# Kernel tuning notes

Hardware: AMD Instinct MI355X
Metric: run time of the kernel (lower is better)

The kernel has to match this reference:

```python
import jax, jax.numpy as jnp
import numpy as np

B, S, D, H = 16, 2048, 2048, 16
HD = D // H
PROJ = D  # proj_ratio = 1.0
PAD_ID = 50257
LN_EPS = 1e-5
MASKED_BIAS = -1e9


def setup_inputs() -> dict:
    key = jax.random.key(0)
    ks = jax.random.split(key, 12)
    sc = 0.02
    return {
        "hidden_states": jax.random.normal(ks[0], (B, S, D), dtype=jnp.float32),
        "input_ids_with_pads": jax.random.randint(ks[1], (B, S), 0, PAD_ID, dtype=jnp.int64),
        "ln_w": jnp.ones((D,), jnp.float32),
        "ln_b": jnp.zeros((D,), jnp.float32),
        "wq": sc * jax.random.normal(ks[2], (D, D), jnp.float32),
        "bq": jnp.zeros((D,), jnp.float32),
        "wk": sc * jax.random.normal(ks[3], (D, D), jnp.float32),
        "bk": jnp.zeros((D,), jnp.float32),
        "wv": sc * jax.random.normal(ks[4], (D, D), jnp.float32),
        "bv": jnp.zeros((D,), jnp.float32),
        "wo": sc * jax.random.normal(ks[5], (D, PROJ), jnp.float32),
        "bo": jnp.zeros((PROJ,), jnp.float32),
    }


def _layernorm(x, g, b):
    mu = jnp.mean(x, axis=-1, keepdims=True)
    var = jnp.mean(jnp.square(x - mu), axis=-1, keepdims=True)
    return (x - mu) * jax.lax.rsqrt(var + LN_EPS) * g + b


def _last_token_index(tokens):
    # select_at_last_token: argmax of cumsum of the non-pad mask == index of
    # the last non-pad token (first index where the cumsum reaches its max).
    mask = (tokens != PAD_ID).astype(jnp.int32)
    return jnp.argmax(jnp.cumsum(mask, axis=1), axis=1)  # [B]


def reference(hidden_states, input_ids_with_pads, ln_w, ln_b,
              wq, bq, wk, bk, wv, bv, wo, bo):
    x = _layernorm(hidden_states, ln_w, ln_b)  # [B,S,D]
    idx = _last_token_index(input_ids_with_pads)
    # Efficient gather instead of the original index_select + diagonal trick.
    x_last = x[jnp.arange(B), idx]  # [B,D]

    q = (x_last @ wq + bq).reshape(B, H, HD)          # single query per batch
    k = (x @ wk + bk).reshape(B, S, H, HD).transpose(0, 2, 1, 3)  # [B,H,S,HD]
    v = (x @ wv + bv).reshape(B, S, H, HD).transpose(0, 2, 1, 3)  # [B,H,S,HD]

    # GPT-Neo _attn: compute in float32, NO 1/sqrt(head_dim) scaling.
    # Causal mask for query at position key_length-1 covers the full key range,
    # i.e. it is all-True here, so it is a no-op (kept implicit).
    w = jnp.einsum("bhd,bhsd->bhs", q.astype(jnp.float32), k.astype(jnp.float32))
    w = jax.nn.softmax(w, axis=-1).astype(v.dtype)    # [B,H,S]
    attn = jnp.einsum("bhs,bhsd->bhd", w, v)          # [B,H,HD]
    attn = attn.reshape(B, D)                          # merge heads
    out = attn @ wo + bo                               # [B,PROJ]
    return out
```

## Files before the change

kernel.cpp:

```cpp
#include <hip/hip_runtime.h>
#include <hip/hip_bf16.h>

#define BB 16
#define SS 2048
#define DD 2048
#define HH 16
#define HDIM 128
#define PAD_ID 50257
#define LN_EPS 1e-5f

__device__ __forceinline__ float block_sum256(float v, float* s4) {
    #pragma unroll
    for (int m = 32; m >= 1; m >>= 1) v += __shfl_xor(v, m, 64);
    __syncthreads();
    if ((threadIdx.x & 63) == 0) s4[threadIdx.x >> 6] = v;
    __syncthreads();
    return s4[0] + s4[1] + s4[2] + s4[3];
}
__device__ __forceinline__ float block_max256(float v, float* s4) {
    #pragma unroll
    for (int m = 32; m >= 1; m >>= 1) v = fmaxf(v, __shfl_xor(v, m, 64));
    __syncthreads();
    if ((threadIdx.x & 63) == 0) s4[threadIdx.x >> 6] = v;
    __syncthreads();
    return fmaxf(fmaxf(s4[0], s4[1]), fmaxf(s4[2], s4[3]));
}

__device__ __forceinline__ void gl16(const float* g, float* l) {
    __builtin_amdgcn_global_load_lds(
        (const __attribute__((address_space(1))) void*)g,
        (__attribute__((address_space(3))) void*)l,
        16, 0, 0);
}

__global__ __launch_bounds__(256) void k_prep(const float* __restrict__ hid, const int* __restrict__ ids,
                                              const float* __restrict__ g, const float* __restrict__ be,
                                              float* __restrict__ xlast) {
    int b = blockIdx.x, t = threadIdx.x;
    __shared__ int sm[256];
    __shared__ float s4[4];
    const int* row = ids + (size_t)b * SS;
    int best = -1;
    for (int s = t; s < SS; s += 256)
        if (row[s] != PAD_ID) best = s;
    sm[t] = best;
    __syncthreads();
    for (int off = 128; off > 0; off >>= 1) {
        if (t < off) sm[t] = max(sm[t], sm[t + off]);
        __syncthreads();
    }
    int idx = (sm[0] < 0) ? 0 : sm[0];
    const float4* row4 = (const float4*)(hid + ((size_t)b * SS + idx) * DD);
    float4 v0 = row4[t], v1 = row4[t + 256];
    float s  = v0.x + v0.y + v0.z + v0.w + v1.x + v1.y + v1.z + v1.w;
    float sq = v0.x*v0.x + v0.y*v0.y + v0.z*v0.z + v0.w*v0.w
             + v1.x*v1.x + v1.y*v1.y + v1.z*v1.z + v1.w*v1.w;
    s  = block_sum256(s, s4);
    sq = block_sum256(sq, s4);
    float mu = s * (1.0f / DD);
    float rstd = rsqrtf(sq * (1.0f / DD) - mu * mu + LN_EPS);
    const float4* g4 = (const float4*)g;
    const float4* b4 = (const float4*)be;
    float4 ga = g4[t], gb = g4[t + 256], ba = b4[t], bb = b4[t + 256];
    float4 o0, o1;
    o0.x = (v0.x - mu) * rstd * ga.x + ba.x;  o0.y = (v0.y - mu) * rstd * ga.y + ba.y;
    o0.z = (v0.z - mu) * rstd * ga.z + ba.z;  o0.w = (v0.w - mu) * rstd * ga.w + ba.w;
    o1.x = (v1.x - mu) * rstd * gb.x + bb.x;  o1.y = (v1.y - mu) * rstd * gb.y + bb.y;
    o1.z = (v1.z - mu) * rstd * gb.z + bb.z;  o1.w = (v1.w - mu) * rstd * gb.w + bb.w;
    ((float4*)(xlast + (size_t)b * DD))[t]       = o0;
    ((float4*)(xlast + (size_t)b * DD))[t + 256] = o1;
}

__global__ __launch_bounds__(256) void k_init3(float* __restrict__ q, float* __restrict__ attn,
                                               float* __restrict__ out, const float* __restrict__ bq,
                                               const float* __restrict__ bv, const float* __restrict__ bo) {
    int i = blockIdx.x * 256 + threadIdx.x;
    int which = blockIdx.y;
    float* dst = which == 0 ? q : (which == 1 ? attn : out);
    const float* bias = which == 0 ? bq : (which == 1 ? bv : bo);
    dst[i] = bias[i & (DD - 1)];
}

__global__ __launch_bounds__(256) void k_q(const float* __restrict__ xlast, const float* __restrict__ wq,
                                           float* __restrict__ q) {
    int ptile = blockIdx.x, kch = blockIdx.y, tid = threadIdx.x;
    __shared__ float xs[16][64];
    {
        int b = tid >> 4, c4 = tid & 15;
        *(float4*)&xs[b][c4 * 4] = *(const float4*)&xlast[(size_t)b * DD + kch * 64 + c4 * 4];
    }
    __syncthreads();
    int p = ptile * 256 + tid;
    float acc[16];
    #pragma unroll
    for (int b = 0; b < 16; b++) acc[b] = 0.f;
    for (int dd = 0; dd < 64; dd++) {
        float wqv = wq[(size_t)(kch * 64 + dd) * DD + p];
        #pragma unroll
        for (int b = 0; b < 16; b++) acc[b] = fmaf(xs[b][dd], wqv, acc[b]);
    }
    #pragma unroll
    for (int b = 0; b < 16; b++) atomicAdd(&q[(size_t)b * DD + p], acc[b]);
}

__global__ __launch_bounds__(256) void k_t(const float* __restrict__ wk, const float* __restrict__ q,
                                           const float* __restrict__ g, float* __restrict__ t_out,
                                           float* __restrict__ tg_out) {
    int d = blockIdx.x, tid = threadIdx.x;
    __shared__ float wkl[16 * 132];
    #pragma unroll
    for (int k = 0; k < 2; k++) {
        int f4 = tid + k * 256;
        int h = f4 >> 5, j4 = f4 & 31;
        *(float4*)&wkl[h * 132 + j4 * 4] = *(const float4*)&wk[(size_t)d * DD + h * 128 + j4 * 4];
    }
    __syncthreads();
    int b = tid >> 4, h = tid & 15;
    const float4* q4 = (const float4*)(q + (size_t)b * DD + h * 128);
    float acc = 0.f;
    #pragma unroll
    for (int j4 = 0; j4 < 32; j4++) {
        float4 qv = q4[j4];
        float4 wv4 = *(const float4*)&wkl[h * 132 + j4 * 4];
        acc = fmaf(qv.x, wv4.x, fmaf(qv.y, wv4.y, fmaf(qv.z, wv4.z, fmaf(qv.w, wv4.w, acc))));
    }
    size_t o = (size_t)(b * 16 + h) * DD + d;
    t_out[o] = acc;
    tg_out[o] = acc * g[d];
}

__global__ __launch_bounds__(256) void k_G(const float* __restrict__ t_in, const float* __restrict__ tg_in,
                                           const float* __restrict__ q, const float* __restrict__ lnb,
                                           const float* __restrict__ bk, float* __restrict__ G1,
                                           float* __restrict__ wconst) {
    int bh = blockIdx.x, tid = threadIdx.x;
    int b = bh >> 4, h = bh & 15;
    __shared__ float s4[4];
    const float4* tg4 = (const float4*)(tg_in + (size_t)bh * DD);
    const float4* t4  = (const float4*)(t_in + (size_t)bh * DD);
    const float4* lb4 = (const float4*)lnb;
    float g1p = 0.f, g2p = 0.f;
    #pragma unroll
    for (int k = 0; k < 2; k++) {
        int f = tid + k * 256;
        float4 a = tg4[f];
        g1p += a.x + a.y + a.z + a.w;
        float4 tv = t4[f];
        float4 bv = lb4[f];
        g2p = fmaf(tv.x, bv.x, fmaf(tv.y, bv.y, fmaf(tv.z, bv.z, fmaf(tv.w, bv.w, g2p))));
    }
    float cp = 0.f;
    if (tid < 128) cp = bk[h * 128 + tid] * q[(size_t)b * DD + h * 128 + tid];
    float G1v = block_sum256(g1p, s4);
    float rest = block_sum256(g2p + cp, s4);
    if (tid == 0) { G1[bh] = G1v; wconst[bh] = rest; }
}

__global__ __launch_bounds__(256) void k_logits8(const float* __restrict__ hid, const float* __restrict__ tg,
                                                 const float* __restrict__ G1, const float* __restrict__ wcst,
                                                 float* __restrict__ wout, float* __restrict__ muA,
                                                 float* __restrict__ rsA) {
    __shared__ float smem[12288];
    int b = blockIdx.x, st = blockIdx.y;
    int tid = threadIdx.x, qd = tid & 15, rp = tid >> 4;
    const float* hb = hid + ((size_t)b * SS + st * 32) * DD;
    const float* tgb = tg + (size_t)b * 16 * DD;

    float raw[2][16], sum[2], ssq[2];
    #pragma unroll
    for (int r = 0; r < 2; r++) {
        sum[r] = 0.f; ssq[r] = 0.f;
        #pragma unroll
        for (int h = 0; h < 16; h++) raw[r][h] = 0.f;
    }

    auto stage = [&](int c, int buf) {
        int d0 = c * 128;
        float* xd = smem + buf * 4096;
        float* td = smem + 8192 + buf * 2048;
        #pragma unroll
        for (int i = 0; i < 4; i++) {
            int f = i * 256 + tid;
            int row = f >> 5, c4 = f & 31;
            gl16(&hb[(size_t)row * DD + d0 + c4 * 4], &xd[f * 4]);
        }
        #pragma unroll
        for (int i = 0; i < 2; i++) {
            int f = i * 256 + tid;
            int h = f >> 5, c4 = f & 31;
            gl16(&tgb[(size_t)h * DD + d0 + c4 * 4], &td[f * 4]);
        }
    };

    stage(0, 0);
    __syncthreads();

    int cur = 0;
    #pragma unroll 1
    for (int c = 0; c < 16; c++) {
        if (c < 15) stage(c + 1, cur ^ 1);
        const float* xb = smem + cur * 4096;
        const float* tb = smem + 8192 + cur * 2048;
        #pragma unroll
        for (int k = 0; k < 2; k++) {
            float4 x0 = *(const float4*)&xb[(rp * 2 + 0) * 128 + (qd + 16 * k) * 4];
            float4 x1 = *(const float4*)&xb[(rp * 2 + 1) * 128 + (qd + 16 * k) * 4];
            #pragma unroll
            for (int h = 0; h < 16; h++) {
                float4 tv = *(const float4*)&tb[h * 128 + (qd + 16 * k) * 4];
                raw[0][h] = fmaf(x0.x, tv.x, fmaf(x0.y, tv.y, fmaf(x0.z, tv.z, fmaf(x0.w, tv.w, raw[0][h]))));
                raw[1][h] = fmaf(x1.x, tv.x, fmaf(x1.y, tv.y, fmaf(x1.z, tv.z, fmaf(x1.w, tv.w, raw[1][h]))));
            }
            sum[0] += x0.x + x0.y + x0.z + x0.w;
            sum[1] += x1.x + x1.y + x1.z + x1.w;
            ssq[0] = fmaf(x0.x, x0.x, fmaf(x0.y, x0.y, fmaf(x0.z, x0.z, fmaf(x0.w, x0.w, ssq[0]))));
            ssq[1] = fmaf(x1.x, x1.x, fmaf(x1.y, x1.y, fmaf(x1.z, x1.z, fmaf(x1.w, x1.w, ssq[1]))));
        }
        __syncthreads();
        cur ^= 1;
    }

    #pragma unroll
    for (int m = 1; m < 16; m <<= 1) {
        #pragma unroll
        for (int r = 0; r < 2; r++) {
            sum[r] += __shfl_xor(sum[r], m, 64);
            ssq[r] += __shfl_xor(ssq[r], m, 64);
        }
    }

    float g1 = G1[b * 16 + qd];
    float wc = wcst[b * 16 + qd];
    float* red = smem;
    #pragma unroll
    for (int rr = 0; rr < 2; rr++) {
        __syncthreads();
        #pragma unroll
        for (int h = 0; h < 16; h++) red[tid * 17 + h] = raw[rr][h];
        __syncthreads();
        float tot = 0.f;
        #pragma unroll
        for (int j = 0; j < 16; j++) tot += red[(rp * 16 + j) * 17 + qd];
        int s = st * 32 + rp * 2 + rr;
        float mu = sum[rr] * (1.0f / DD);
        float rstd = rsqrtf(ssq[rr] * (1.0f / DD) - mu * mu + LN_EPS);
        wout[(size_t)(b * 16 + qd) * SS + s] = rstd * (tot - mu * g1) + wc;
        if (qd == 0) { muA[(size_t)b * SS + s] = mu; rsA[(size_t)b * SS + s] = rstd; }
    }
}

__global__ __launch_bounds__(256) void k_softmax(const float* __restrict__ wlog, const float* __restrict__ muA,
                                                 const float* __restrict__ rsA, float* __restrict__ coef,
                                                 float* __restrict__ Mout) {
    int bh = blockIdx.x, tid = threadIdx.x;
    int b = bh >> 4;
    __shared__ float s4[4];
    const float4* w4 = (const float4*)(wlog + (size_t)bh * SS);
    float4 v0 = w4[tid], v1 = w4[tid + 256];
    float mx = fmaxf(fmaxf(fmaxf(v0.x, v0.y), fmaxf(v0.z, v0.w)),
                     fmaxf(fmaxf(v1.x, v1.y), fmaxf(v1.z, v1.w)));
    mx = block_max256(mx, s4);
    float4 e0, e1;
    e0.x = __expf(v0.x - mx); e0.y = __expf(v0.y - mx); e0.z = __expf(v0.z - mx); e0.w = __expf(v0.w - mx);
    e1.x = __expf(v1.x - mx); e1.y = __expf(v1.y - mx); e1.z = __expf(v1.z - mx); e1.w = __expf(v1.w - mx);
    float ssum = e0.x + e0.y + e0.z + e0.w + e1.x + e1.y + e1.z + e1.w;
    ssum = block_sum256(ssum, s4);
    float inv = 1.0f / ssum;
    const float4* r4 = (const float4*)(rsA + (size_t)b * SS);
    const float4* m4 = (const float4*)(muA + (size_t)b * SS);
    float4 ra = r4[tid], rb = r4[tid + 256], ma = m4[tid], mb = m4[tid + 256];
    float4 c0, c1;
    c0.x = e0.x * inv * ra.x; c0.y = e0.y * inv * ra.y; c0.z = e0.z * inv * ra.z; c0.w = e0.w * inv * ra.w;
    c1.x = e1.x * inv * rb.x; c1.y = e1.y * inv * rb.y; c1.z = e1.z * inv * rb.z; c1.w = e1.w * inv * rb.w;
    ((float4*)(coef + (size_t)bh * SS))[tid] = c0;
    ((float4*)(coef + (size_t)bh * SS))[tid + 256] = c1;
    float Mp = c0.x * ma.x + c0.y * ma.y + c0.z * ma.z + c0.w * ma.w
             + c1.x * mb.x + c1.y * mb.y + c1.z * mb.z + c1.w * mb.w;
    Mp = block_sum256(Mp, s4);
    if (tid == 0) Mout[bh] = Mp;
}

__global__ __launch_bounds__(256) void k_pv6(const float* __restrict__ hid, const float* __restrict__ coef,
                                             float* __restrict__ Apart) {
    int b = blockIdx.x, dt = blockIdx.y, ch = blockIdx.z, tid = threadIdx.x;
    __shared__ float cl[128][16];
    int s0 = ch * 128;
    #pragma unroll
    for (int k = 0; k < 2; k++) {
        int f = tid + k * 256; int h = f >> 5, s4i = f & 31;
        float4 c4 = *(const float4*)&coef[(size_t)(b * 16 + h) * SS + s0 + s4i * 4];
        cl[s4i * 4 + 0][h] = c4.x; cl[s4i * 4 + 1][h] = c4.y;
        cl[s4i * 4 + 2][h] = c4.z; cl[s4i * 4 + 3][h] = c4.w;
    }
    __syncthreads();
    int d = dt * 1024 + tid * 4;
    const float* hb = hid + ((size_t)b * SS + s0) * DD + d;
    float4 acc[16];
    #pragma unroll
    for (int h = 0; h < 16; h++) acc[h] = make_float4(0.f, 0.f, 0.f, 0.f);
    float4 xv[8];
    #pragma unroll
    for (int i = 0; i < 8; i++) xv[i] = *(const float4*)(hb + (size_t)i * DD);
    #pragma unroll 1
    for (int sb = 0; sb < 16; sb++) {
        #pragma unroll
        for (int i = 0; i < 8; i++) {
            int s = sb * 8 + i;
            float4 x = xv[i];
            if (sb < 15) xv[i] = *(const float4*)(hb + (size_t)(s + 8) * DD);
            float4 ca = *(const float4*)&cl[s][0];
            float4 cb = *(const float4*)&cl[s][4];
            float4 cc = *(const float4*)&cl[s][8];
            float4 cd = *(const float4*)&cl[s][12];
            acc[0].x = fmaf(ca.x, x.x, acc[0].x); acc[0].y = fmaf(ca.x, x.y, acc[0].y);
            acc[0].z = fmaf(ca.x, x.z, acc[0].z); acc[0].w = fmaf(ca.x, x.w, acc[0].w);
            acc[1].x = fmaf(ca.y, x.x, acc[1].x); acc[1].y = fmaf(ca.y, x.y, acc[1].y);
            acc[1].z = fmaf(ca.y, x.z, acc[1].z); acc[1].w = fmaf(ca.y, x.w, acc[1].w);
            acc[2].x = fmaf(ca.z, x.x, acc[2].x); acc[2].y = fmaf(ca.z, x.y, acc[2].y);
            acc[2].z = fmaf(ca.z, x.z, acc[2].z); acc[2].w = fmaf(ca.z, x.w, acc[2].w);
            acc[3].x = fmaf(ca.w, x.x, acc[3].x); acc[3].y = fmaf(ca.w, x.y, acc[3].y);
            acc[3].z = fmaf(ca.w, x.z, acc[3].z); acc[3].w = fmaf(ca.w, x.w, acc[3].w);
            acc[4].x = fmaf(cb.x, x.x, acc[4].x); acc[4].y = fmaf(cb.x, x.y, acc[4].y);
            acc[4].z = fmaf(cb.x, x.z, acc[4].z); acc[4].w = fmaf(cb.x, x.w, acc[4].w);
            acc[5].x = fmaf(cb.y, x.x, acc[5].x); acc[5].y = fmaf(cb.y, x.y, acc[5].y);
            acc[5].z = fmaf(cb.y, x.z, acc[5].z); acc[5].w = fmaf(cb.y, x.w, acc[5].w);
            acc[6].x = fmaf(cb.z, x.x, acc[6].x); acc[6].y = fmaf(cb.z, x.y, acc[6].y);
            acc[6].z = fmaf(cb.z, x.z, acc[6].z); acc[6].w = fmaf(cb.z, x.w, acc[6].w);
            acc[7].x = fmaf(cb.w, x.x, acc[7].x); acc[7].y = fmaf(cb.w, x.y, acc[7].y);
            acc[7].z = fmaf(cb.w, x.z, acc[7].z); acc[7].w = fmaf(cb.w, x.w, acc[7].w);
            acc[8].x = fmaf(cc.x, x.x, acc[8].x); acc[8].y = fmaf(cc.x, x.y, acc[8].y);
            acc[8].z = fmaf(cc.x, x.z, acc[8].z); acc[8].w = fmaf(cc.x, x.w, acc[8].w);
            acc[9].x = fmaf(cc.y, x.x, acc[9].x); acc[9].y = fmaf(cc.y, x.y, acc[9].y);
            acc[9].z = fmaf(cc.y, x.z, acc[9].z); acc[9].w = fmaf(cc.y, x.w, acc[9].w);
            acc[10].x = fmaf(cc.z, x.x, acc[10].x); acc[10].y = fmaf(cc.z, x.y, acc[10].y);
            acc[10].z = fmaf(cc.z, x.z, acc[10].z); acc[10].w = fmaf(cc.z, x.w, acc[10].w);
            acc[11].x = fmaf(cc.w, x.x, acc[11].x); acc[11].y = fmaf(cc.w, x.y, acc[11].y);
            acc[11].z = fmaf(cc.w, x.z, acc[11].z); acc[11].w = fmaf(cc.w, x.w, acc[11].w);
            acc[12].x = fmaf(cd.x, x.x, acc[12].x); acc[12].y = fmaf(cd.x, x.y, acc[12].y);
            acc[12].z = fmaf(cd.x, x.z, acc[12].z); acc[12].w = fmaf(cd.x, x.w, acc[12].w);
            acc[13].x = fmaf(cd.y, x.x, acc[13].x); acc[13].y = fmaf(cd.y, x.y, acc[13].y);
            acc[13].z = fmaf(cd.y, x.z, acc[13].z); acc[13].w = fmaf(cd.y, x.w, acc[13].w);
            acc[14].x = fmaf(cd.z, x.x, acc[14].x); acc[14].y = fmaf(cd.z, x.y, acc[14].y);
            acc[14].z = fmaf(cd.z, x.z, acc[14].z); acc[14].w = fmaf(cd.z, x.w, acc[14].w);
            acc[15].x = fmaf(cd.w, x.x, acc[15].x); acc[15].y = fmaf(cd.w, x.y, acc[15].y);
            acc[15].z = fmaf(cd.w, x.z, acc[15].z); acc[15].w = fmaf(cd.w, x.w, acc[15].w);
        }
    }
    #pragma unroll
    for (int h = 0; h < 16; h++)
        *(float4*)&Apart[((size_t)(ch * 16 + b) * 16 + h) * DD + d] = acc[h];
}

__global__ __launch_bounds__(256) void k_attnv(const float* __restrict__ Apart, const float* __restrict__ M,
                                               const float* __restrict__ g, const float* __restrict__ be,
                                               const float* __restrict__ wv, float* __restrict__ attn) {
    int h = blockIdx.x, dc = blockIdx.y, tid = threadIdx.x;
    __shared__ float yl[16][64];
    int d0 = dc * 64;
    {
        int b = tid >> 4, c4 = tid & 15;
        float4 a4 = make_float4(0.f, 0.f, 0.f, 0.f);
        #pragma unroll
        for (int ch = 0; ch < 16; ch++) {
            float4 v = *(const float4*)&Apart[((size_t)(ch * 16 + b) * 16 + h) * DD + d0 + c4 * 4];
            a4.x += v.x; a4.y += v.y; a4.z += v.z; a4.w += v.w;
        }
        float4 g4 = *(const float4*)&g[d0 + c4 * 4];
        float4 b4 = *(const float4*)&be[d0 + c4 * 4];
        float m = M[b * 16 + h];
        float4 y;
        y.x = g4.x * (a4.x - m) + b4.x;  y.y = g4.y * (a4.y - m) + b4.y;
        y.z = g4.z * (a4.z - m) + b4.z;  y.w = g4.w * (a4.w - m) + b4.w;
        *(float4*)&yl[b][c4 * 4] = y;
    }
    __syncthreads();
    int j = tid & 127, h2 = tid >> 7;
    float acc[16];
    #pragma unroll
    for (int b = 0; b < 16; b++) acc[b] = 0.f;
    for (int dl = 0; dl < 32; dl++) {
        int dd = h2 * 32 + dl;
        float wvv = wv[(size_t)(d0 + dd) * DD + h * 128 + j];
        #pragma unroll
        for (int b = 0; b < 16; b++) acc[b] = fmaf(yl[b][dd], wvv, acc[b]);
    }
    #pragma unroll
    for (int b = 0; b < 16; b++) atomicAdd(&attn[(size_t)b * DD + h * 128 + j], acc[b]);
}

__global__ __launch_bounds__(256) void k_out(const float* __restrict__ attn, const float* __restrict__ wo,
                                             float* __restrict__ out) {
    int ptile = blockIdx.x, cch = blockIdx.y, tid = threadIdx.x;
    __shared__ float al[16][64];
    int c0 = cch * 64;
    {
        int b = tid >> 4, c4 = tid & 15;
        *(float4*)&al[b][c4 * 4] = *(const float4*)&attn[(size_t)b * DD + c0 + c4 * 4];
    }
    __syncthreads();
    int p = ptile * 256 + tid;
    float acc[16];
    #pragma unroll
    for (int b = 0; b < 16; b++) acc[b] = 0.f;
    for (int cc = 0; cc < 64; cc++) {
        float wov = wo[(size_t)(c0 + cc) * DD + p];
        #pragma unroll
        for (int b = 0; b < 16; b++) acc[b] = fmaf(al[b][cc], wov, acc[b]);
    }
    #pragma unroll
    for (int b = 0; b < 16; b++) atomicAdd(&out[(size_t)b * DD + p], acc[b]);
}

extern "C" void kernel_launch(void* const* d_in, const int* in_sizes, int n_in,
                              void* d_out, int out_size, void* d_ws, size_t ws_size,
                              hipStream_t stream) {
    const float* hid = (const float*)d_in[0];
    const int*   ids = (const int*)d_in[1];
    const float* lnw = (const float*)d_in[2];
    const float* lnb = (const float*)d_in[3];
    const float* wq  = (const float*)d_in[4];
    const float* bq  = (const float*)d_in[5];
    const float* wk  = (const float*)d_in[6];
    const float* bk  = (const float*)d_in[7];
    const float* wv  = (const float*)d_in[8];
    const float* bv  = (const float*)d_in[9];
    const float* wo  = (const float*)d_in[10];
    const float* bo  = (const float*)d_in[11];
    float* out = (float*)d_out;

    float* ws = (float*)d_ws;
    float* xlast = ws;
    float* q     = xlast + 32768;
    float* t     = q + 32768;
    float* tg    = t + 524288;
    float* G1    = tg + 524288;
    float* wcst  = G1 + 256;
    float* wlog  = wcst + 256;
    float* muA   = wlog + 524288;
    float* rsA   = muA + 32768;
    float* coef  = rsA + 32768;
    float* Mbh   = coef + 524288;
    float* Abh   = Mbh + 256;
    float* attn  = Abh + 524288;
    float* Apart = attn + 32768;

    k_prep<<<16, 256, 0, stream>>>(hid, ids, lnw, lnb, xlast);
    k_init3<<<dim3(128, 3), 256, 0, stream>>>(q, attn, out, bq, bv, bo);
    k_q<<<dim3(8, 32), 256, 0, stream>>>(xlast, wq, q);
    k_t<<<2048, 256, 0, stream>>>(wk, q, lnw, t, tg);
    k_G<<<256, 256, 0, stream>>>(t, tg, q, lnb, bk, G1, wcst);
    k_logits8<<<dim3(16, 64), 256, 0, stream>>>(hid, tg, G1, wcst, wlog, muA, rsA);
    k_softmax<<<256, 256, 0, stream>>>(wlog, muA, rsA, coef, Mbh);
    k_pv6<<<dim3(16, 2, 16), 256, 0, stream>>>(hid, coef, Apart);
    k_attnv<<<dim3(16, 32), 256, 0, stream>>>(Apart, Mbh, lnw, lnb, wv, attn);
    k_out<<<dim3(8, 32), 256, 0, stream>>>(attn, wo, out);
}
```

Measured before the change: 222.6 us.

## Retile logits kernel to 8 rows by 4 heads per thread

Changes the per-thread register tile in the logits kernel from 2 sequence rows × 16 heads to 8 rows × 4 heads. Each thread now loads 4 head vectors and 8 row vectors per step, which changes the ratio of LDS traffic to FMAs. The cross-lane reduction moves from a padded shared-memory transpose to shuffle reductions, followed by a small shared-memory scatter for the output. Only one head group computes the LayerNorm statistics, so the redundant sum and sum-of-squares work is dropped. The tradeoff is many more shuffle reductions per thread and more divergent branching.

```diff
diff --git a/kernel.cpp b/kernel.cpp
--- a/kernel.cpp
+++ b/kernel.cpp
@@ -156,22 +156,23 @@
     if (tid == 0) { G1[bh] = G1v; wconst[bh] = rest; }
 }
 
-__global__ __launch_bounds__(256) void k_logits8(const float* __restrict__ hid, const float* __restrict__ tg,
-                                                 const float* __restrict__ G1, const float* __restrict__ wcst,
-                                                 float* __restrict__ wout, float* __restrict__ muA,
-                                                 float* __restrict__ rsA) {
+__global__ __launch_bounds__(256) void k_logits13(const float* __restrict__ hid, const float* __restrict__ tg,
+                                                  const float* __restrict__ G1, const float* __restrict__ wcst,
+                                                  float* __restrict__ wout, float* __restrict__ muA,
+                                                  float* __restrict__ rsA) {
     __shared__ float smem[12288];
     int b = blockIdx.x, st = blockIdx.y;
-    int tid = threadIdx.x, qd = tid & 15, rp = tid >> 4;
+    int tid = threadIdx.x, qd = tid & 15, g = tid >> 4;
+    int sg = g & 3, hg = g >> 2;
     const float* hb = hid + ((size_t)b * SS + st * 32) * DD;
     const float* tgb = tg + (size_t)b * 16 * DD;
 
-    float raw[2][16], sum[2], ssq[2];
-    #pragma unroll
-    for (int r = 0; r < 2; r++) {
+    float raw[8][4], sum[8], ssq[8];
+    #pragma unroll
+    for (int r = 0; r < 8; r++) {
         sum[r] = 0.f; ssq[r] = 0.f;
         #pragma unroll
-        for (int h = 0; h < 16; h++) raw[r][h] = 0.f;
+        for (int h = 0; h < 4; h++) raw[r][h] = 0.f;
     }
 
     auto stage = [&](int c, int buf) {
@@ -203,18 +204,33 @@
         const float* tb = smem + 8192 + cur * 2048;
         #pragma unroll
         for (int k = 0; k < 2; k++) {
-            float4 x0 = *(const float4*)&xb[(rp * 2 + 0) * 128 + (qd + 16 * k) * 4];
-            float4 x1 = *(const float4*)&xb[(rp * 2 + 1) * 128 + (qd + 16 * k) * 4];
+            float4 tv0 = *(const float4*)&tb[(hg * 4 + 0) * 128 + (qd + 16 * k) * 4];
+            float4 tv1 = *(const float4*)&tb[(hg * 4 + 1) * 128 + (qd + 16 * k) * 4];
+            float4 tv2 = *(const float4*)&tb[(hg * 4 + 2) * 128 + (qd + 16 * k) * 4];
+            float4 tv3 = *(const float4*)&tb[(hg * 4 + 3) * 128 + (qd + 16 * k) * 4];
             #pragma unroll
-            for (int h = 0; h < 16; h++) {
-                float4 tv = *(const float4*)&tb[h * 128 + (qd + 16 * k) * 4];
-                raw[0][h] = fmaf(x0.x, tv.x, fmaf(x0.y, tv.y, fmaf(x0.z, tv.z, fmaf(x0.w, tv.w, raw[0][h]))));
-                raw[1][h] = fmaf(x1.x, tv.x, fmaf(x1.y, tv.y, fmaf(x1.z, tv.z, fmaf(x1.w, tv.w, raw[1][h]))));
+            for (int half = 0; half < 2; half++) {
+                float4 xr[4];
+                #pragma unroll
+                for (int r2 = 0; r2 < 4; r2++)
+                    xr[r2] = *(const float4*)&xb[(sg * 8 + half * 4 + r2) * 128 + (qd + 16 * k) * 4];
+                #pragma unroll
+                for (int r2 = 0; r2 < 4; r2++) {
+                    float4 x = xr[r2];
+                    raw[half * 4 + r2][0] = fmaf(x.x, tv0.x, fmaf(x.y, tv0.y, fmaf(x.z, tv0.z, fmaf(x.w, tv0.w, raw[half * 4 + r2][0]))));
+                    raw[half * 4 + r2][1] = fmaf(x.x, tv1.x, fmaf(x.y, tv1.y, fmaf(x.z, tv1.z, fmaf(x.w, tv1.w, raw[half * 4 + r2][1]))));
+                    raw[half * 4 + r2][2] = fmaf(x.x, tv2.x, fmaf(x.y, tv2.y, fmaf(x.z, tv2.z, fmaf(x.w, tv2.w, raw[half * 4 + r2][2]))));
+                    raw[half * 4 + r2][3] = fmaf(x.x, tv3.x, fmaf(x.y, tv3.y, fmaf(x.z, tv3.z, fmaf(x.w, tv3.w, raw[half * 4 + r2][3]))));
+                }
+                if (hg == 0) {
+                    #pragma unroll
+                    for (int r2 = 0; r2 < 4; r2++) {
+                        float4 x = xr[r2];
+                        sum[half * 4 + r2] += x.x + x.y + x.z + x.w;
+                        ssq[half * 4 + r2] = fmaf(x.x, x.x, fmaf(x.y, x.y, fmaf(x.z, x.z, fmaf(x.w, x.w, ssq[half * 4 + r2]))));
+                    }
+                }
             }
-            sum[0] += x0.x + x0.y + x0.z + x0.w;
-            sum[1] += x1.x + x1.y + x1.z + x1.w;
-            ssq[0] = fmaf(x0.x, x0.x, fmaf(x0.y, x0.y, fmaf(x0.z, x0.z, fmaf(x0.w, x0.w, ssq[0]))));
-            ssq[1] = fmaf(x1.x, x1.x, fmaf(x1.y, x1.y, fmaf(x1.z, x1.z, fmaf(x1.w, x1.w, ssq[1]))));
         }
         __syncthreads();
         cur ^= 1;
@@ -223,29 +239,47 @@
     #pragma unroll
     for (int m = 1; m < 16; m <<= 1) {
         #pragma unroll
-        for (int r = 0; r < 2; r++) {
+        for (int r = 0; r < 8; r++) {
+            #pragma unroll
+            for (int h = 0; h < 4; h++) raw[r][h] += __shfl_xor(raw[r][h], m, 64);
             sum[r] += __shfl_xor(sum[r], m, 64);
             ssq[r] += __shfl_xor(ssq[r], m, 64);
         }
     }
 
-    float g1 = G1[b * 16 + qd];
-    float wc = wcst[b * 16 + qd];
-    float* red = smem;
-    #pragma unroll
-    for (int rr = 0; rr < 2; rr++) {
-        __syncthreads();
-        #pragma unroll
-        for (int h = 0; h < 16; h++) red[tid * 17 + h] = raw[rr][h];
-        __syncthreads();
-        float tot = 0.f;
-        #pragma unroll
-        for (int j = 0; j < 16; j++) tot += red[(rp * 16 + j) * 17 + qd];
-        int s = st * 32 + rp * 2 + rr;
-        float mu = sum[rr] * (1.0f / DD);
-        float rstd = rsqrtf(ssq[rr] * (1.0f / DD) - mu * mu + LN_EPS);
-        wout[(size_t)(b * 16 + qd) * SS + s] = rstd * (tot - mu * g1) + wc;
-        if (qd == 0) { muA[(size_t)b * SS + s] = mu; rsA[(size_t)b * SS + s] = rstd; }
+    float* rawsm = smem;
+    float* musm  = smem + 544;
+    float* rssm  = smem + 576;
+    if (qd == 0) {
+        #pragma unroll
+        for (int r = 0; r < 8; r++)
+            #pragma unroll
+            for (int h = 0; h < 4; h++)
+                rawsm[g * 32 + r * 4 + h] = raw[r][h];
+    }
+    if (hg == 0 && qd == 0) {
+        #pragma unroll
+        for (int r = 0; r < 8; r++) {
+            int sl = sg * 8 + r;
+            float mu = sum[r] * (1.0f / DD);
+            float rstd = rsqrtf(ssq[r] * (1.0f / DD) - mu * mu + LN_EPS);
+            musm[sl] = mu; rssm[sl] = rstd;
+            muA[(size_t)b * SS + st * 32 + sl] = mu;
+            rsA[(size_t)b * SS + st * 32 + sl] = rstd;
+        }
+    }
+    __syncthreads();
+    #pragma unroll
+    for (int io = 0; io < 2; io++) {
+        int v = tid + io * 256;
+        int g2 = v >> 5, idx = v & 31;
+        int rr2 = idx >> 2, hh2 = idx & 3;
+        int head = (g2 >> 2) * 4 + hh2;
+        int sl = (g2 & 3) * 8 + rr2;
+        float val = rawsm[g2 * 32 + idx];
+        float mu2 = musm[sl], rs2 = rssm[sl];
+        wout[(size_t)(b * 16 + head) * SS + st * 32 + sl] =
+            rs2 * (val - mu2 * G1[b * 16 + head]) + wcst[b * 16 + head];
     }
 }
 
@@ -449,7 +483,7 @@
     k_q<<<dim3(8, 32), 256, 0, stream>>>(xlast, wq, q);
     k_t<<<2048, 256, 0, stream>>>(wk, q, lnw, t, tg);
     k_G<<<256, 256, 0, stream>>>(t, tg, q, lnb, bk, G1, wcst);
-    k_logits8<<<dim3(16, 64), 256, 0, stream>>>(hid, tg, G1, wcst, wlog, muA, rsA);
+    k_logits13<<<dim3(16, 64), 256, 0, stream>>>(hid, tg, G1, wcst, wlog, muA, rsA);
     k_softmax<<<256, 256, 0, stream>>>(wlog, muA, rsA, coef, Mbh);
     k_pv6<<<dim3(16, 2, 16), 256, 0, stream>>>(hid, coef, Apart);
     k_attnv<<<dim3(16, 32), 256, 0, stream>>>(Apart, Mbh, lnw, lnb, wv, attn);
```

Measured after the change: 227.6 us. +2.3%, slower.
